# Kernel tuning notes

Hardware: AMD Instinct MI355X
Metric: run time of the kernel (lower is better)

The kernel has to match this reference:

```python
import jax, jax.numpy as jnp
import numpy as np


def setup_inputs() -> dict:
    key = jax.random.key(0)
    ks = jax.random.split(key, 12)
    N_DRUGS, D, N_CELLS, C_IN, E = 4096, 128, 1024, 1000, 500000
    inp = {
        "drug_hidden_out": jax.random.normal(ks[0], (N_DRUGS, D), dtype=jnp.float32),
        "cell_hidden_out": jax.random.normal(ks[1], (N_CELLS, C_IN), dtype=jnp.float32),
        # columns: drug1_idx, drug2_idx, cell_idx, label (original code indexes
        # drug_hidden_out with ALL THREE index columns, so bound by N_DRUGS)
        "all_edges": jax.random.randint(ks[2], (E, 4), 0, N_DRUGS, dtype=jnp.int64),
        # proj: Linear(1000, 128)
        "proj_W": jax.random.normal(ks[3], (D, C_IN), dtype=jnp.float32) * 0.03,
        "proj_b": jnp.zeros((D,), dtype=jnp.float32),
        # NN: Linear(128,32) -> ReLU -> Linear(32,32) -> ReLU -> Linear(32,32)
        #     -> ReLU -> Dropout(eval=identity) -> Linear(32,1) -> Sigmoid
        "W1": jax.random.normal(ks[4], (32, D), dtype=jnp.float32) * 0.08,
        "b1": jnp.zeros((32,), dtype=jnp.float32),
        "W2": jax.random.normal(ks[5], (32, 32), dtype=jnp.float32) * 0.17,
        "b2": jnp.zeros((32,), dtype=jnp.float32),
        "W3": jax.random.normal(ks[6], (32, 32), dtype=jnp.float32) * 0.17,
        "b3": jnp.zeros((32,), dtype=jnp.float32),
        "W4": jax.random.normal(ks[7], (1, 32), dtype=jnp.float32) * 0.17,
        "b4": jnp.zeros((1,), dtype=jnp.float32),
    }
    return inp


def reference(drug_hidden_out, cell_hidden_out, all_edges,
              proj_W, proj_b, W1, b1, W2, b2, W3, b3, W4, b4):
    # proj is computed in the original forward but its result is never used
    # downstream (the code re-indexes drug_hidden_out for cell_fea).
    _cell_proj = cell_hidden_out @ proj_W.T + proj_b  # [n_cells, 128], dead value

    edges = all_edges.T                 # [4, E]
    label = edges[3]                    # [E]
    edge_index = edges[:3]              # [3, E]

    drug1_fea = drug_hidden_out[edge_index[0]]   # [E, 128] gather
    drug2_fea = drug_hidden_out[edge_index[1]]   # [E, 128] gather
    cell_fea = drug_hidden_out[edge_index[2]]    # [E, 128] gather (faithful to source bug)
    logits = drug1_fea * drug2_fea * cell_fea    # [E, 128]

    h = jax.nn.relu(logits @ W1.T + b1)          # [E, 32]
    h = jax.nn.relu(h @ W2.T + b2)               # [E, 32]
    h = jax.nn.relu(h @ W3.T + b3)               # [E, 32] (dropout = identity in eval)
    x = jax.nn.sigmoid(h @ W4.T + b4)            # [E, 1]
    return x, label
```

## Files before the change

kernel.cpp:

```cpp
#include <hip/hip_runtime.h>
#include <stdint.h>

#define DD 128
#define HH 32
#define RS 36
#define TABQ (4096 * DD / 4)
#define BLOB_OFF (1u << 20)

typedef _Float16 f16;
typedef _Float16 f16x4 __attribute__((ext_vector_type(4)));
typedef _Float16 f16x8 __attribute__((ext_vector_type(8)));
typedef float    f32x4 __attribute__((ext_vector_type(4)));

#define GL1(p)  ((const __attribute__((address_space(1))) void*)(p))
#define LDS3(p) ((__attribute__((address_space(3))) void*)(p))

__global__ __launch_bounds__(256)
void synergy_prepass(const float* __restrict__ drug,
                     const float* __restrict__ W1, const float* __restrict__ W2,
                     const float* __restrict__ W3, const float* __restrict__ W4,
                     f16* __restrict__ tab)
{
    const int tid = threadIdx.x;
    if ((int)blockIdx.x == 512) {
        f16x8* __restrict__ blob16 = (f16x8*)((char*)tab + BLOB_OFF);
        const float4* __restrict__ W1v = (const float4*)W1;
        #pragma unroll
        for (int p = 0; p < 2; ++p) {
            const int S = p * 256 + tid;
            const int t = S >> 8, f = (S >> 6) & 3, l = S & 63;
            const int mm = l & 15, qq = l >> 4;
            const int c4 = (t * 16 + mm) * (DD / 4) + f * 8 + qq * 2;
            const float4 w0 = W1v[c4], w1 = W1v[c4 + 1];
            f16x8 r;
            r[0]=(f16)w0.x; r[1]=(f16)w0.y; r[2]=(f16)w0.z; r[3]=(f16)w0.w;
            r[4]=(f16)w1.x; r[5]=(f16)w1.y; r[6]=(f16)w1.z; r[7]=(f16)w1.w;
            blob16[S] = r;
        }
        {
            const int B = tid & 127;
            const int t = B >> 6, l = B & 63;
            const int mm = l & 15, qq = l >> 4;
            const int c4 = (t * 16 + mm) * (HH / 4) + qq * 2;
            const float4* __restrict__ src = (tid < 128) ? (const float4*)W2 : (const float4*)W3;
            const float4 w0 = src[c4], w1 = src[c4 + 1];
            f16x8 r;
            r[0]=(f16)w0.x; r[1]=(f16)w0.y; r[2]=(f16)w0.z; r[3]=(f16)w0.w;
            r[4]=(f16)w1.x; r[5]=(f16)w1.y; r[6]=(f16)w1.z; r[7]=(f16)w1.w;
            blob16[512 + (tid & 128) + B] = r;
        }
        if (tid < 64) {
            const int mm = tid & 15, qq = tid >> 4;
            f16x8 r;
            #pragma unroll
            for (int j = 0; j < 8; ++j)
                r[j] = (mm == 0) ? (f16)W4[qq * 8 + j] : (f16)0.0f;
            blob16[768 + tid] = r;
        }
        return;
    }
    const int i = blockIdx.x * 256 + tid;
    if (i < TABQ) {
        const float4 v = ((const float4*)drug)[i];
        f16x4 h;
        h[0]=(f16)v.x; h[1]=(f16)v.y; h[2]=(f16)v.z; h[3]=(f16)v.w;
        ((f16x4*)tab)[i] = h;
    }
}

__global__ __launch_bounds__(256, 3)
void synergy_main(const f16* __restrict__ tab, const int* __restrict__ edges,
                  const float* __restrict__ b1, const float* __restrict__ b2,
                  const float* __restrict__ b3, const float* __restrict__ b4,
                  float* __restrict__ out, int E, int NG)
{
    __shared__ __align__(16) f16 stage[4][6144];
    __shared__ __align__(16) f16 hbuf[4][16 * RS];

    const int tid  = threadIdx.x;
    const int wave = tid >> 6;
    const int lane = tid & 63;
    const int m    = lane & 15;
    const int q    = lane >> 4;

    const int WSTR = (int)gridDim.x * 4;
    int g = (int)blockIdx.x * 4 + wave;
    if (g >= NG) return;

    const char* __restrict__ tabB   = (const char*)tab;
    const int4* __restrict__ edges4 = (const int4*)edges;

    const f16x8* __restrict__ blobG = (const f16x8*)(tabB + BLOB_OFF);
    f16x8 wa[2][4];
    #pragma unroll
    for (int t = 0; t < 2; ++t)
        #pragma unroll
        for (int f = 0; f < 4; ++f)
            wa[t][f] = blobG[(t * 4 + f) * 64 + lane];
    const f16x8 w2a = blobG[512 + lane], w2b = blobG[576 + lane];
    const f16x8 w3a = blobG[640 + lane], w3b = blobG[704 + lane];
    const f16x8 wf4 = blobG[768 + lane];
    const float b1a = b1[m], b1b = b1[16 + m];
    const float b2a = b2[m], b2b = b2[16 + m];
    const float b3a = b3[m], b3b = b3[16 + m];
    const float b4v = b4[0];

    f16* __restrict__ stg = stage[wave];
    f16* __restrict__ hb  = hbuf[wave];

    auto load_ed = [&](int gg) -> int4 {
        int e = (gg << 4) + m;
        e = (e < E) ? e : (E - 1);
        return edges4[e];
    };
    auto issue_dma = [&](const int4 ed) {
        int rowb[12];
        #pragma unroll
        for (int gg = 0; gg < 4; ++gg) {
            const int src = 4 * gg + q;
            rowb[0 * 4 + gg] = __shfl(ed.x, src, 64) << 8;
            rowb[1 * 4 + gg] = __shfl(ed.y, src, 64) << 8;
            rowb[2 * 4 + gg] = __shfl(ed.z, src, 64) << 8;
        }
        __builtin_amdgcn_sched_barrier(0);
        #pragma unroll
        for (int t = 0; t < 3; ++t)
            #pragma unroll
            for (int gg = 0; gg < 4; ++gg) {
                const int seg16 = ((m + 4 * gg + q) & 15) << 4;
                __builtin_amdgcn_global_load_lds(
                    GL1(tabB + (size_t)(rowb[t * 4 + gg] + seg16)),
                    LDS3((char*)stg + (t * 16 + 4 * gg) * 256), 16, 0, 0);
            }
    };

    int4 ed_cur = load_ed(g);
    issue_dma(ed_cur);
    int gn = g + WSTR;
    int4 ed_nxt = load_ed((gn < NG) ? gn : g);

    for (;;) {
        __builtin_amdgcn_s_waitcnt(0x0F70);
        __builtin_amdgcn_sched_barrier(0);

        f32x4 acc0 = {b1a, b1a, b1a, b1a};
        f32x4 acc1 = {b1b, b1b, b1b, b1b};
        #pragma unroll
        for (int f = 0; f < 4; ++f) {
            const int slot = (((f * 4 + q) - m) & 15) << 3;
            const f16x8 v0 = *(const f16x8*)(stg + (0 * 16 + m) * 128 + slot);
            const f16x8 v1 = *(const f16x8*)(stg + (1 * 16 + m) * 128 + slot);
            const f16x8 v2 = *(const f16x8*)(stg + (2 * 16 + m) * 128 + slot);
            const f16x8 p = v0 * v1 * v2;
            acc0 = __builtin_amdgcn_mfma_f32_16x16x32_f16(p, wa[0][f], acc0, 0, 0, 0);
            acc1 = __builtin_amdgcn_mfma_f32_16x16x32_f16(p, wa[1][f], acc1, 0, 0, 0);
        }
        #pragma unroll
        for (int r = 0; r < 4; ++r) {
            const int row = 4 * q + r;
            hb[row * RS + m]      = (f16)fmaxf(acc0[r], 0.0f);
            hb[row * RS + 16 + m] = (f16)fmaxf(acc1[r], 0.0f);
        }

        const int gf = gn + WSTR;
        const int4 ed_fut = load_ed((gf < NG) ? gf : g);

        {
            const f16x8 a2 = *(const f16x8*)(hb + m * RS + q * 8);
            f32x4 c0 = {b2a, b2a, b2a, b2a};
            f32x4 c1 = {b2b, b2b, b2b, b2b};
            c0 = __builtin_amdgcn_mfma_f32_16x16x32_f16(a2, w2a, c0, 0, 0, 0);
            c1 = __builtin_amdgcn_mfma_f32_16x16x32_f16(a2, w2b, c1, 0, 0, 0);
            #pragma unroll
            for (int r = 0; r < 4; ++r) {
                const int row = 4 * q + r;
                hb[row * RS + m]      = (f16)fmaxf(c0[r], 0.0f);
                hb[row * RS + 16 + m] = (f16)fmaxf(c1[r], 0.0f);
            }
        }

        {
            const f16x8 a3 = *(const f16x8*)(hb + m * RS + q * 8);
            f32x4 d0 = {b3a, b3a, b3a, b3a};
            f32x4 d1 = {b3b, b3b, b3b, b3b};
            d0 = __builtin_amdgcn_mfma_f32_16x16x32_f16(a3, w3a, d0, 0, 0, 0);
            d1 = __builtin_amdgcn_mfma_f32_16x16x32_f16(a3, w3b, d1, 0, 0, 0);
            #pragma unroll
            for (int r = 0; r < 4; ++r) {
                const int row = 4 * q + r;
                hb[row * RS + m]      = (f16)fmaxf(d0[r], 0.0f);
                hb[row * RS + 16 + m] = (f16)fmaxf(d1[r], 0.0f);
            }
        }

        {
            const f16x8 a4 = *(const f16x8*)(hb + m * RS + q * 8);
            f32x4 z = {b4v, b4v, b4v, b4v};
            z = __builtin_amdgcn_mfma_f32_16x16x32_f16(a4, wf4, z, 0, 0, 0);
            if (m == 0) {
                const int e0 = (g << 4) + 4 * q;
                float4 res;
                res.x = 1.0f / (1.0f + __expf(-z[0]));
                res.y = 1.0f / (1.0f + __expf(-z[1]));
                res.z = 1.0f / (1.0f + __expf(-z[2]));
                res.w = 1.0f / (1.0f + __expf(-z[3]));
                if (e0 + 3 < E) *(float4*)(out + e0) = res;
                else {
                    if (e0 + 0 < E) out[e0 + 0] = res.x;
                    if (e0 + 1 < E) out[e0 + 1] = res.y;
                    if (e0 + 2 < E) out[e0 + 2] = res.z;
                }
            }
        }
        const int eL = (g << 4) + lane;
        if (lane < 16 && eL < E) out[E + eL] = (float)ed_cur.w;

        if (gn >= NG) break;
        issue_dma(ed_nxt);
        g = gn; gn = gf; ed_cur = ed_nxt; ed_nxt = ed_fut;
    }
}

extern "C" void kernel_launch(void* const* d_in, const int* in_sizes, int n_in,
                              void* d_out, int out_size, void* d_ws, size_t ws_size,
                              hipStream_t stream)
{
    const float* drug  = (const float*)d_in[0];
    const int*   edges = (const int*)d_in[2];
    const float* W1 = (const float*)d_in[5];
    const float* b1 = (const float*)d_in[6];
    const float* W2 = (const float*)d_in[7];
    const float* b2 = (const float*)d_in[8];
    const float* W3 = (const float*)d_in[9];
    const float* b3 = (const float*)d_in[10];
    const float* W4 = (const float*)d_in[11];
    const float* b4 = (const float*)d_in[12];
    float* out = (float*)d_out;
    f16*   tab = (f16*)d_ws;

    const int E  = in_sizes[2] / 4;
    const int NG = (E + 15) / 16;

    hipLaunchKernelGGL(synergy_prepass, dim3(513), dim3(256), 0, stream,
                       drug, W1, W2, W3, W4, tab);
    int blocks = (NG + 3) / 4;
    if (blocks > 768) blocks = 768;
    hipLaunchKernelGGL(synergy_main, dim3(blocks), dim3(256), 0, stream,
                       tab, edges, b1, b2, b3, b4, out, E, NG);
}
```

Before: 122.9 us.

## Gather drug rows directly into registers and move W1 fragments to LDS

The async global-to-LDS staging of the three gathered drug rows, with its swizzled LDS reads, is replaced by direct per-lane 16-byte global loads that land in the MFMA A-operand layout. The next group's gather is issued right after layer 1, so it overlaps layers 2-4. The W1 weight fragments move from registers to a block-shared LDS array, which frees VGPRs for the register-held gather buffer. Occupancy is raised to 4 blocks per CU and the grid cap to 1024 blocks. The gathered data now sits in registers across the later layers, which trades an LDS round trip for register pressure and a shorter prefetch distance.

After: 156.2 us. +27.1%, slower.

```diff
diff --git a/kernel.cpp b/kernel.cpp
--- a/kernel.cpp
+++ b/kernel.cpp
@@ -11,9 +11,6 @@
 typedef _Float16 f16x4 __attribute__((ext_vector_type(4)));
 typedef _Float16 f16x8 __attribute__((ext_vector_type(8)));
 typedef float    f32x4 __attribute__((ext_vector_type(4)));
-
-#define GL1(p)  ((const __attribute__((address_space(1))) void*)(p))
-#define LDS3(p) ((__attribute__((address_space(3))) void*)(p))
 
 __global__ __launch_bounds__(256)
 void synergy_prepass(const float* __restrict__ drug,
@@ -68,13 +65,13 @@
     }
 }
 
-__global__ __launch_bounds__(256, 3)
+__global__ __launch_bounds__(256, 4)
 void synergy_main(const f16* __restrict__ tab, const int* __restrict__ edges,
                   const float* __restrict__ b1, const float* __restrict__ b2,
                   const float* __restrict__ b3, const float* __restrict__ b4,
                   float* __restrict__ out, int E, int NG)
 {
-    __shared__ __align__(16) f16 stage[4][6144];
+    __shared__ __align__(16) f16x8 w1lds[512];
     __shared__ __align__(16) f16 hbuf[4][16 * RS];
 
     const int tid  = threadIdx.x;
@@ -83,20 +80,19 @@
     const int m    = lane & 15;
     const int q    = lane >> 4;
 
+    const char* __restrict__ tabB   = (const char*)tab;
+    const f16x8* __restrict__ blobG = (const f16x8*)(tabB + BLOB_OFF);
+
+    w1lds[tid]       = blobG[tid];
+    w1lds[256 + tid] = blobG[256 + tid];
+    __syncthreads();
+
     const int WSTR = (int)gridDim.x * 4;
     int g = (int)blockIdx.x * 4 + wave;
     if (g >= NG) return;
 
-    const char* __restrict__ tabB   = (const char*)tab;
     const int4* __restrict__ edges4 = (const int4*)edges;
 
-    const f16x8* __restrict__ blobG = (const f16x8*)(tabB + BLOB_OFF);
-    f16x8 wa[2][4];
-    #pragma unroll
-    for (int t = 0; t < 2; ++t)
-        #pragma unroll
-        for (int f = 0; f < 4; ++f)
-            wa[t][f] = blobG[(t * 4 + f) * 64 + lane];
     const f16x8 w2a = blobG[512 + lane], w2b = blobG[576 + lane];
     const f16x8 w3a = blobG[640 + lane], w3b = blobG[704 + lane];
     const f16x8 wf4 = blobG[768 + lane];
@@ -105,55 +101,42 @@
     const float b3a = b3[m], b3b = b3[16 + m];
     const float b4v = b4[0];
 
-    f16* __restrict__ stg = stage[wave];
-    f16* __restrict__ hb  = hbuf[wave];
+    f16* __restrict__ hb = hbuf[wave];
 
     auto load_ed = [&](int gg) -> int4 {
         int e = (gg << 4) + m;
         e = (e < E) ? e : (E - 1);
         return edges4[e];
     };
-    auto issue_dma = [&](const int4 ed) {
-        int rowb[12];
-        #pragma unroll
-        for (int gg = 0; gg < 4; ++gg) {
-            const int src = 4 * gg + q;
-            rowb[0 * 4 + gg] = __shfl(ed.x, src, 64) << 8;
-            rowb[1 * 4 + gg] = __shfl(ed.y, src, 64) << 8;
-            rowb[2 * 4 + gg] = __shfl(ed.z, src, 64) << 8;
-        }
-        __builtin_amdgcn_sched_barrier(0);
-        #pragma unroll
-        for (int t = 0; t < 3; ++t)
-            #pragma unroll
-            for (int gg = 0; gg < 4; ++gg) {
-                const int seg16 = ((m + 4 * gg + q) & 15) << 4;
-                __builtin_amdgcn_global_load_lds(
-                    GL1(tabB + (size_t)(rowb[t * 4 + gg] + seg16)),
-                    LDS3((char*)stg + (t * 16 + 4 * gg) * 256), 16, 0, 0);
-            }
+
+    f16x8 v[4][3];
+    auto issue_gather = [&](const int4 ed) {
+        const char* __restrict__ p0 = tabB + ((ed.x << 8) | (q << 4));
+        const char* __restrict__ p1 = tabB + ((ed.y << 8) | (q << 4));
+        const char* __restrict__ p2 = tabB + ((ed.z << 8) | (q << 4));
+        #pragma unroll
+        for (int f = 0; f < 4; ++f) {
+            v[f][0] = *(const f16x8*)(p0 + f * 64);
+            v[f][1] = *(const f16x8*)(p1 + f * 64);
+            v[f][2] = *(const f16x8*)(p2 + f * 64);
+        }
     };
 
     int4 ed_cur = load_ed(g);
-    issue_dma(ed_cur);
+    issue_gather(ed_cur);
     int gn = g + WSTR;
     int4 ed_nxt = load_ed((gn < NG) ? gn : g);
 
     for (;;) {
-        __builtin_amdgcn_s_waitcnt(0x0F70);
-        __builtin_amdgcn_sched_barrier(0);
-
         f32x4 acc0 = {b1a, b1a, b1a, b1a};
         f32x4 acc1 = {b1b, b1b, b1b, b1b};
         #pragma unroll
         for (int f = 0; f < 4; ++f) {
-            const int slot = (((f * 4 + q) - m) & 15) << 3;
-            const f16x8 v0 = *(const f16x8*)(stg + (0 * 16 + m) * 128 + slot);
-            const f16x8 v1 = *(const f16x8*)(stg + (1 * 16 + m) * 128 + slot);
-            const f16x8 v2 = *(const f16x8*)(stg + (2 * 16 + m) * 128 + slot);
-            const f16x8 p = v0 * v1 * v2;
-            acc0 = __builtin_amdgcn_mfma_f32_16x16x32_f16(p, wa[0][f], acc0, 0, 0, 0);
-            acc1 = __builtin_amdgcn_mfma_f32_16x16x32_f16(p, wa[1][f], acc1, 0, 0, 0);
+            const f16x8 wa0 = w1lds[f * 64 + lane];
+            const f16x8 wa1 = w1lds[256 + f * 64 + lane];
+            const f16x8 p = v[f][0] * v[f][1] * v[f][2];
+            acc0 = __builtin_amdgcn_mfma_f32_16x16x32_f16(p, wa0, acc0, 0, 0, 0);
+            acc1 = __builtin_amdgcn_mfma_f32_16x16x32_f16(p, wa1, acc1, 0, 0, 0);
         }
         #pragma unroll
         for (int r = 0; r < 4; ++r) {
@@ -162,8 +145,13 @@
             hb[row * RS + 16 + m] = (f16)fmaxf(acc1[r], 0.0f);
         }
 
-        const int gf = gn + WSTR;
-        const int4 ed_fut = load_ed((gf < NG) ? gf : g);
+        const bool last = (gn >= NG);
+        int4 ed_fut = ed_nxt;
+        if (!last) {
+            issue_gather(ed_nxt);
+            const int gf = gn + WSTR;
+            ed_fut = load_ed((gf < NG) ? gf : g);
+        }
 
         {
             const f16x8 a2 = *(const f16x8*)(hb + m * RS + q * 8);
@@ -215,9 +203,8 @@
         const int eL = (g << 4) + lane;
         if (lane < 16 && eL < E) out[E + eL] = (float)ed_cur.w;
 
-        if (gn >= NG) break;
-        issue_dma(ed_nxt);
-        g = gn; gn = gf; ed_cur = ed_nxt; ed_nxt = ed_fut;
+        if (last) break;
+        g = gn; gn += WSTR; ed_cur = ed_nxt; ed_nxt = ed_fut;
     }
 }
 
@@ -244,7 +231,7 @@
     hipLaunchKernelGGL(synergy_prepass, dim3(513), dim3(256), 0, stream,
                        drug, W1, W2, W3, W4, tab);
     int blocks = (NG + 3) / 4;
-    if (blocks > 768) blocks = 768;
+    if (blocks > 1024) blocks = 1024;
     hipLaunchKernelGGL(synergy_main, dim3(blocks), dim3(256), 0, stream,
                        tab, edges, b1, b2, b3, b4, out, E, NG);
 }
```
